# Kernel optimization log

Hardware: AMD Instinct MI355X
Metric: run time of the kernel (lower is better)

Reference implementation:

```python
import jax, jax.numpy as jnp
import numpy as np

STRIDE = 2
PAD = 1


def _deform_conv2d(x, offset, mask, weight, bias):
    # Modulated deformable conv2d (torchvision semantics), offset_groups=1,
    # stride=2, padding=1, dilation=1, groups=1.
    B, C, H, W = x.shape
    Cout, Cin, kH, kW = weight.shape
    K = kH * kW
    _, _, Ho, Wo = mask.shape

    off = offset.reshape(B, K, 2, Ho, Wo)  # [:, :, 0]=dy, [:, :, 1]=dx
    ii = jnp.repeat(jnp.arange(kH), kW).astype(x.dtype)  # [K] kernel row index
    jj = jnp.tile(jnp.arange(kW), kH).astype(x.dtype)    # [K] kernel col index
    gy = (jnp.arange(Ho) * STRIDE - PAD).astype(x.dtype)  # [Ho] base y of output pixel
    gx = (jnp.arange(Wo) * STRIDE - PAD).astype(x.dtype)  # [Wo] base x

    # Fractional sampling positions per (batch, kernel point, out pixel): [B,K,Ho,Wo]
    py = off[:, :, 0] + gy[None, None, :, None] + ii[None, :, None, None]
    px = off[:, :, 1] + gx[None, None, None, :] + jj[None, :, None, None]

    y0 = jnp.floor(py)
    x0 = jnp.floor(px)
    dy = py - y0
    dx = px - x0

    xf = x.reshape(B, C, H * W)

    def gather(yc, xc):
        # Bilinear corner gather with zero padding outside the image.
        valid = (yc >= 0) & (yc <= H - 1) & (xc >= 0) & (xc <= W - 1)
        yi = jnp.clip(yc, 0, H - 1).astype(jnp.int32)
        xi = jnp.clip(xc, 0, W - 1).astype(jnp.int32)
        idx = (yi * W + xi).reshape(B, 1, K * Ho * Wo)
        g = jnp.take_along_axis(xf, jnp.broadcast_to(idx, (B, C, K * Ho * Wo)), axis=2)
        return g.reshape(B, C, K, Ho, Wo) * valid[:, None].astype(x.dtype)

    w00 = ((1 - dy) * (1 - dx))[:, None]
    w01 = ((1 - dy) * dx)[:, None]
    w10 = (dy * (1 - dx))[:, None]
    w11 = (dy * dx)[:, None]

    val = (gather(y0, x0) * w00 + gather(y0, x0 + 1) * w01
           + gather(y0 + 1, x0) * w10 + gather(y0 + 1, x0 + 1) * w11)
    val = val * mask[:, None]  # modulation: [B,C,K,Ho,Wo] * [B,1,K,Ho,Wo]

    out = jnp.einsum('bckhw,ock->bohw', val, weight.reshape(Cout, Cin, K))
    return out + bias[None, :, None, None]


def setup_inputs() -> dict:
    key = jax.random.key(0)
    k1, k2, k3, k4, k5 = jax.random.split(key, 5)
    B, C, H, W = 8, 128, 128, 128
    Cout, kH, kW = 128, 3, 3
    Ho = (H + 2 * PAD - kH) // STRIDE + 1
    Wo = (W + 2 * PAD - kW) // STRIDE + 1
    x = jax.random.normal(k1, (B, C, H, W), dtype=jnp.float32)
    offset = jax.random.normal(k2, (B, 2 * kH * kW, Ho, Wo), dtype=jnp.float32)
    mask = jax.random.uniform(k3, (B, kH * kW, Ho, Wo), dtype=jnp.float32)
    weight = jax.random.normal(k4, (Cout, C, kH, kW), dtype=jnp.float32)
    bias = jax.random.normal(k5, (Cout,), dtype=jnp.float32)
    return {"x": x, "offset": offset, "mask": mask, "weight": weight, "bias": bias}


def reference(x, offset, mask, weight, bias):
    return _deform_conv2d(x, offset, mask, weight, bias)
```

## Files before the change

### kernel.cpp

```cpp
#include <hip/hip_runtime.h>
#include <hip/hip_bf16.h>

typedef __attribute__((ext_vector_type(8))) short short8;
typedef __attribute__((ext_vector_type(4))) short short4v;
typedef __attribute__((ext_vector_type(4))) float f32x4;
typedef __attribute__((ext_vector_type(4))) int int4v;
typedef unsigned long long u64;

#define HH 128
#define WW 128
#define CC 128
#define COUT 128
#define HO 64
#define WO 64
#define KK 9
#define PXB 64
#define NREC (KK * PXB)

__device__ __forceinline__ unsigned short bf16bits(float f) {
    union { float f; unsigned u; } u; u.f = f;
    unsigned r = u.u + 0x7fffu + ((u.u >> 16) & 1u);
    return (unsigned short)(r >> 16);
}
__device__ __forceinline__ float b2f(unsigned short h) {
    union { unsigned u; float f; } v; v.u = ((unsigned)h) << 16; return v.f;
}

__global__ void wprep_kernel(const float* __restrict__ w, unsigned short* __restrict__ wp) {
    int i = blockIdx.x * 256 + threadIdx.x;
    if (i >= KK * COUT * CC) return;
    int kp = i / (COUT * CC);
    int r = i - kp * (COUT * CC);
    int o = r >> 7;
    int c = r & 127;
    wp[i] = bf16bits(w[((size_t)o * CC + c) * KK + kp]);
}

__global__ __launch_bounds__(256, 4)
void xt_kernel(const float* __restrict__ x, unsigned short* __restrict__ xt) {
    const int bi = blockIdx.x;
    const int b = bi >> 7;
    const int y = bi & 127;
    const int t = threadIdx.x;
    __shared__ unsigned short tile[128][132];

    const float* src = x + (((size_t)b * CC) * HH + y) * WW;
#pragma unroll 8
    for (int c0 = 0; c0 < CC; c0 += 2) {
        int c = c0 + (t >> 7);
        int xx = t & 127;
        tile[xx][c] = bf16bits(src[(size_t)c * (HH * WW) + xx]);
    }
    __syncthreads();
    unsigned short* dst = xt + (((size_t)b * HH + y) * WW) * CC;
#pragma unroll
    for (int it = 0; it < 4; ++it) {
        int lin = it * 256 + t;
        int xx = lin >> 3;
        int cb = (lin & 7) * 16;
        const u64* lp = (const u64*)&tile[xx][cb];
        u64* op = (u64*)(dst + (size_t)xx * CC + cb);
        op[0] = lp[0]; op[1] = lp[1]; op[2] = lp[2]; op[3] = lp[3];
    }
}

__global__ __launch_bounds__(256, 8)
void add_kernel(float* __restrict__ out, const float* __restrict__ p1) {
    size_t i = ((size_t)blockIdx.x * 256 + threadIdx.x) * 4;
    const size_t N = (size_t)8 * COUT * HO * WO;
    const size_t STR = (size_t)2048 * 256 * 4;
    for (; i < N; i += STR) {
        f32x4 a = *(const f32x4*)(out + i);
        f32x4 b = *(const f32x4*)(p1 + i);
        a = a + b;
        *(f32x4*)(out + i) = a;
    }
}

template <bool SPLIT>
__global__ __launch_bounds__(256, 4)
void dcn14_kernel(const unsigned short* __restrict__ xt, const float* __restrict__ offset,
                  const float* __restrict__ mask, const unsigned short* __restrict__ wprep,
                  const float* __restrict__ bias, float* __restrict__ out,
                  float* __restrict__ part1) {
    const int blk = blockIdx.x;
    const int b = blk & 7;
    const int ho = (blk >> 3) & 63;
    const int chalf = SPLIT ? (blk >> 9) : 0;
    const int t = threadIdx.x;
    const int lane = t & 63;
    const int wid = t >> 6;

    __shared__ int            s_cidx[NREC][4];
    __shared__ float          s_w[NREC][4];
    __shared__ unsigned short s_val[PXB][72];

    for (int e = t; e < NREC; e += 256) {
        int kp = e >> 6;
        int wo = e & 63;
        int ky = kp / 3, kx = kp - ky * 3;
        float dy = offset[(((size_t)b * 18 + 2 * kp    ) * HO + ho) * WO + wo];
        float dx = offset[(((size_t)b * 18 + 2 * kp + 1) * HO + ho) * WO + wo];
        float m  = mask  [(((size_t)b * 9  + kp        ) * HO + ho) * WO + wo];
        float py = dy + (float)(2 * ho - 1 + ky);
        float px = dx + (float)(2 * wo - 1 + kx);
        float fy0 = floorf(py), fx0 = floorf(px);
        float ay = py - fy0, ax = px - fx0;
        int y0 = (int)fy0, x0 = (int)fx0;
        int y1 = y0 + 1, x1 = x0 + 1;
        bool vy0 = (unsigned)y0 < HH, vy1 = (unsigned)y1 < HH;
        bool vx0 = (unsigned)x0 < WW, vx1 = (unsigned)x1 < WW;
        float w00 = (vy0 && vx0) ? (1.f - ay) * (1.f - ax) * m : 0.f;
        float w01 = (vy0 && vx1) ? (1.f - ay) * ax * m : 0.f;
        float w10 = (vy1 && vx0) ? ay * (1.f - ax) * m : 0.f;
        float w11 = (vy1 && vx1) ? ay * ax * m : 0.f;
        int cy0 = min(max(y0, 0), HH - 1), cy1 = min(max(y1, 0), HH - 1);
        int cx0 = min(max(x0, 0), WW - 1), cx1 = min(max(x1, 0), WW - 1);
        s_cidx[e][0] = (cy0 * WW + cx0) * CC;
        s_cidx[e][1] = (cy0 * WW + cx1) * CC;
        s_cidx[e][2] = (cy1 * WW + cx0) * CC;
        s_cidx[e][3] = (cy1 * WW + cx1) * CC;
        s_w[e][0] = w00; s_w[e][1] = w01; s_w[e][2] = w10; s_w[e][3] = w11;
    }

    f32x4 acc[2][4];
#pragma unroll
    for (int i = 0; i < 2; ++i)
#pragma unroll
        for (int j = 0; j < 4; ++j) acc[i][j] = (f32x4){0.f, 0.f, 0.f, 0.f};

    const int o_base = wid * 32;
    const int l16 = lane & 15;
    const int lhi = lane >> 4;

    const unsigned short* xtb = xt + (size_t)b * (HH * WW * CC);
    const int gpx = t >> 2;
    const int gcb = (t & 3) * 16;

    const int cbeg = SPLIT ? chalf * 64 : 0;
    const int cend = SPLIT ? cbeg + 64 : CC;

    for (int c0 = cbeg; c0 < cend; c0 += 64) {
        for (int kp = 0; kp < KK; ++kp) {
            __syncthreads();

            int rec = kp * PXB + gpx;
            int4v ci = *(const int4v*)&s_cidx[rec][0];
            f32x4 wq = *(const f32x4*)&s_w[rec][0];
            const unsigned short* bp = xtb + c0 + gcb;
            short8 h00a = *(const short8*)(bp + ci.x);
            short8 h00b = *(const short8*)(bp + ci.x + 8);
            short8 h01a = *(const short8*)(bp + ci.y);
            short8 h01b = *(const short8*)(bp + ci.y + 8);
            short8 h10a = *(const short8*)(bp + ci.z);
            short8 h10b = *(const short8*)(bp + ci.z + 8);
            short8 h11a = *(const short8*)(bp + ci.w);
            short8 h11b = *(const short8*)(bp + ci.w + 8);

            const unsigned short* wb = wprep + (size_t)kp * (COUT * CC) + c0 + lhi * 8;
            short8 afr[2][2];
#pragma unroll
            for (int mr = 0; mr < 2; ++mr)
#pragma unroll
                for (int kk = 0; kk < 2; ++kk)
                    afr[mr][kk] = *(const short8*)(wb + (size_t)(o_base + mr * 16 + l16) * CC + kk * 32);

            short8 v0, v1;
#pragma unroll
            for (int j = 0; j < 8; ++j) {
                float val = wq.x * b2f((unsigned short)h00a[j]) + wq.y * b2f((unsigned short)h01a[j])
                          + wq.z * b2f((unsigned short)h10a[j]) + wq.w * b2f((unsigned short)h11a[j]);
                v0[j] = (short)bf16bits(val);
            }
#pragma unroll
            for (int j = 0; j < 8; ++j) {
                float val = wq.x * b2f((unsigned short)h00b[j]) + wq.y * b2f((unsigned short)h01b[j])
                          + wq.z * b2f((unsigned short)h10b[j]) + wq.w * b2f((unsigned short)h11b[j]);
                v1[j] = (short)bf16bits(val);
            }
            *(short8*)&s_val[gpx][gcb] = v0;
            *(short8*)&s_val[gpx][gcb + 8] = v1;

            __syncthreads();

#pragma unroll
            for (int nr = 0; nr < 4; ++nr) {
                short8 bfr[2];
#pragma unroll
                for (int kk = 0; kk < 2; ++kk)
                    bfr[kk] = *(const short8*)&s_val[nr * 16 + l16][kk * 32 + lhi * 8];
#pragma unroll
                for (int mr = 0; mr < 2; ++mr)
#pragma unroll
                    for (int kk = 0; kk < 2; ++kk)
                        acc[mr][nr] = __builtin_amdgcn_mfma_f32_16x16x32_bf16(
                            afr[mr][kk], bfr[kk], acc[mr][nr], 0, 0, 0);
            }
        }
    }

    float* dst = (SPLIT && chalf == 1) ? part1 : out;
    const bool addb = (!SPLIT) || (chalf == 0);
    float* ob = dst + ((size_t)b * COUT) * (HO * WO) + (size_t)ho * WO;
#pragma unroll
    for (int mr = 0; mr < 2; ++mr) {
        int o_r = o_base + mr * 16 + lhi * 4;
#pragma unroll
        for (int r = 0; r < 4; ++r) {
            int o = o_r + r;
            float bs = addb ? bias[o] : 0.f;
#pragma unroll
            for (int nr = 0; nr < 4; ++nr) {
                int wo = nr * 16 + l16;
                ob[(size_t)o * (HO * WO) + wo] = acc[mr][nr][r] + bs;
            }
        }
    }
}

#define PXB6 32
#define NREC6 (KK * PXB6)
template <bool PREP>
__global__ __launch_bounds__(256, 4)
void dcn6_kernel(const float* __restrict__ x, const float* __restrict__ offset,
                 const float* __restrict__ mask, const float* __restrict__ weight,
                 const unsigned short* __restrict__ wprep,
                 const float* __restrict__ bias, float* __restrict__ out) {
    const int blk = blockIdx.x;
    const int b = blk & 7;
    const int rr = blk >> 3;
    const int ho = rr >> 1;
    const int px0 = (rr & 1) * PXB6;
    const int t = threadIdx.x;
    const int lane = t & 63;
    const int wid = t >> 6;

    __shared__ int            s_off[NREC6][2];
    __shared__ float          s_wq[NREC6][4];
    __shared__ unsigned short s_wt6[COUT][40];
    __shared__ unsigned short s_val6[PXB6][40];

    for (int e = t; e < NREC6; e += 256) {
        int kp = e >> 5;
        int wo = px0 + (e & 31);
        int ky = kp / 3, kx = kp - ky * 3;
        float dy = offset[(((size_t)b * 18 + 2 * kp    ) * HO + ho) * WO + wo];
        float dx = offset[(((size_t)b * 18 + 2 * kp + 1) * HO + ho) * WO + wo];
        float m  = mask  [(((size_t)b * 9  + kp        ) * HO + ho) * WO + wo];
        float py = dy + (float)(2 * ho - 1 + ky);
        float px = dx + (float)(2 * wo - 1 + kx);
        float fy0 = floorf(py), fx0 = floorf(px);
        float ay = py - fy0, ax = px - fx0;
        int y0 = (int)fy0, x0 = (int)fx0;
        int y1 = y0 + 1, x1 = x0 + 1;
        bool vy0 = (unsigned)y0 < HH, vy1 = (unsigned)y1 < HH;
        bool vx0 = (unsigned)x0 < WW, vx1 = (unsigned)x1 < WW;
        float w00 = (vy0 && vx0) ? (1.f - ay) * (1.f - ax) * m : 0.f;
        float w01 = (vy0 && vx1) ? (1.f - ay) * ax * m : 0.f;
        float w10 = (vy1 && vx0) ? ay * (1.f - ax) * m : 0.f;
        float w11 = (vy1 && vx1) ? ay * ax * m : 0.f;
        int bx = min(max(x0, 0), WW - 2);
        float wA0 = (x0 == bx     ? w00 : 0.f) + (x1 == bx     ? w01 : 0.f);
        float wB0 = (x0 == bx + 1 ? w00 : 0.f) + (x1 == bx + 1 ? w01 : 0.f);
        float wA1 = (x0 == bx     ? w10 : 0.f) + (x1 == bx     ? w11 : 0.f);
        float wB1 = (x0 == bx + 1 ? w10 : 0.f) + (x1 == bx + 1 ? w11 : 0.f);
        int cy0 = min(max(y0, 0), HH - 1), cy1 = min(max(y1, 0), HH - 1);
        s_off[e][0] = cy0 * WW + bx;
        s_off[e][1] = cy1 * WW + bx;
        s_wq[e][0] = wA0; s_wq[e][1] = wB0; s_wq[e][2] = wA1; s_wq[e][3] = wB1;
    }

    f32x4 acc[2][2];
#pragma unroll
    for (int i = 0; i < 2; ++i)
#pragma unroll
        for (int j = 0; j < 2; ++j) acc[i][j] = (f32x4){0.f, 0.f, 0.f, 0.f};

    const int o_base = wid * 32;
    const int l16 = lane & 15;
    const int lhi = lane >> 4;
    const float* xb = x + (size_t)b * CC * HH * WW;
    const int gpx = t & 31;
    const int gcg = t >> 5;

    for (int c0 = 0; c0 < CC; c0 += 32) {
        for (int kp = 0; kp < KK; ++kp) {
            __syncthreads();
            if (PREP) {
                const unsigned short* src =
                    wprep + ((size_t)kp * COUT + (t >> 1)) * CC + c0 + (t & 1) * 16;
                short8 w0 = *(const short8*)(src);
                short8 w1 = *(const short8*)(src + 8);
                *(short8*)&s_wt6[t >> 1][(t & 1) * 16] = w0;
                *(short8*)&s_wt6[t >> 1][(t & 1) * 16 + 8] = w1;
            } else {
                int o = t & 127;
                int clb = (t >> 7) * 16;
                const float* wp = weight + (size_t)o * (CC * KK) + (size_t)(c0 + clb) * KK + kp;
                short8 w0, w1;
#pragma unroll
                for (int j = 0; j < 8; ++j) w0[j] = (short)bf16bits(wp[j * KK]);
#pragma unroll
                for (int j = 0; j < 8; ++j) w1[j] = (short)bf16bits(wp[(8 + j) * KK]);
                *(short8*)&s_wt6[o][clb] = w0;
                *(short8*)&s_wt6[o][clb + 8] = w1;
            }
            {
                int rec = kp * PXB6 + gpx;
                int o0 = s_off[rec][0], o1 = s_off[rec][1];
                f32x4 wq = *(const f32x4*)&s_wq[rec][0];
                const float* pl = xb + (size_t)(c0 + gcg * 4) * (HH * WW);
                short4v v;
#pragma unroll
                for (int j = 0; j < 4; ++j) {
                    const float* p = pl + (size_t)j * (HH * WW);
                    float2 f0 = *(const float2*)(p + o0);
                    float2 f1 = *(const float2*)(p + o1);
                    float val = wq.x * f0.x + wq.y * f0.y + wq.z * f1.x + wq.w * f1.y;
                    v[j] = (short)bf16bits(val);
                }
                *(short4v*)&s_val6[gpx][gcg * 4] = v;
            }
            __syncthreads();
            short8 afr[2];
#pragma unroll
            for (int mr = 0; mr < 2; ++mr)
                afr[mr] = *(const short8*)&s_wt6[o_base + mr * 16 + l16][lhi * 8];
            short8 bfr[2];
#pragma unroll
            for (int nr = 0; nr < 2; ++nr)
                bfr[nr] = *(const short8*)&s_val6[nr * 16 + l16][lhi * 8];
#pragma unroll
            for (int mr = 0; mr < 2; ++mr)
#pragma unroll
                for (int nr = 0; nr < 2; ++nr)
                    acc[mr][nr] = __builtin_amdgcn_mfma_f32_16x16x32_bf16(
                        afr[mr], bfr[nr], acc[mr][nr], 0, 0, 0);
        }
    }

    float* ob = out + ((size_t)b * COUT) * (HO * WO) + (size_t)ho * WO;
#pragma unroll
    for (int mr = 0; mr < 2; ++mr) {
        int o_r = o_base + mr * 16 + lhi * 4;
#pragma unroll
        for (int r = 0; r < 4; ++r) {
            int o = o_r + r;
            float bs = bias[o];
#pragma unroll
            for (int nr = 0; nr < 2; ++nr) {
                int wo = px0 + nr * 16 + l16;
                ob[(size_t)o * (HO * WO) + wo] = acc[mr][nr][r] + bs;
            }
        }
    }
}

extern "C" void kernel_launch(void* const* d_in, const int* in_sizes, int n_in,
                              void* d_out, int out_size, void* d_ws, size_t ws_size,
                              hipStream_t stream) {
    (void)in_sizes; (void)n_in; (void)out_size;
    const float* x      = (const float*)d_in[0];
    const float* offset = (const float*)d_in[1];
    const float* mask   = (const float*)d_in[2];
    const float* weight = (const float*)d_in[3];
    const float* bias   = (const float*)d_in[4];
    float* out = (float*)d_out;

    const size_t wbytes  = (size_t)KK * COUT * CC * sizeof(unsigned short);
    const size_t xtoff   = (size_t)1 << 20;
    const size_t xtbytes = (size_t)8 * HH * WW * CC * sizeof(unsigned short);
    const size_t p1off   = xtoff + xtbytes;
    const size_t p1bytes = (size_t)8 * COUT * HO * WO * sizeof(float);

    if (ws_size >= p1off + p1bytes) {
        unsigned short* wp  = (unsigned short*)d_ws;
        unsigned short* xtp = (unsigned short*)((char*)d_ws + xtoff);
        float* p1           = (float*)((char*)d_ws + p1off);
        wprep_kernel<<<dim3((KK * COUT * CC + 255) / 256), dim3(256), 0, stream>>>(weight, wp);
        xt_kernel<<<dim3(1024), dim3(256), 0, stream>>>(x, xtp);
        dcn14_kernel<true><<<dim3(1024), dim3(256), 0, stream>>>(xtp, offset, mask, wp, bias, out, p1);
        add_kernel<<<dim3(2048), dim3(256), 0, stream>>>(out, p1);
    } else if (ws_size >= xtoff + xtbytes) {
        unsigned short* wp  = (unsigned short*)d_ws;
        unsigned short* xtp = (unsigned short*)((char*)d_ws + xtoff);
        wprep_kernel<<<dim3((KK * COUT * CC + 255) / 256), dim3(256), 0, stream>>>(weight, wp);
        xt_kernel<<<dim3(1024), dim3(256), 0, stream>>>(x, xtp);
        dcn14_kernel<false><<<dim3(512), dim3(256), 0, stream>>>(xtp, offset, mask, wp, bias, out, nullptr);
    } else if (ws_size >= wbytes) {
        unsigned short* wp = (unsigned short*)d_ws;
        wprep_kernel<<<dim3((KK * COUT * CC + 255) / 256), dim3(256), 0, stream>>>(weight, wp);
        dcn6_kernel<true><<<dim3(1024), dim3(256), 0, stream>>>(x, offset, mask, weight, wp, bias, out);
    } else {
        dcn6_kernel<false><<<dim3(1024), dim3(256), 0, stream>>>(x, offset, mask, weight, nullptr, bias, out);
    }
}
```

Before: 70.50 us.

## Merge prep kernels and replace partial-sum add pass with atomic accumulation

Folds the weight conversion, x transpose, and zeroing of the output into a single prep launch. The split-channel DCN kernel then accumulates both channel halves directly into the output with float atomicAdd, which removes the separate partial buffer and the add kernel. This cuts two launches and a full read/write pass over the output. In exchange it adds an explicit zero-fill of the output, atomic traffic, and nondeterministic summation order. The wprep fallback path is also changed to use the unprepared dcn6 variant.

```diff
diff --git a/kernel.cpp b/kernel.cpp
--- a/kernel.cpp
+++ b/kernel.cpp
@@ -26,63 +26,58 @@
     union { unsigned u; float f; } v; v.u = ((unsigned)h) << 16; return v.f;
 }
 
-__global__ void wprep_kernel(const float* __restrict__ w, unsigned short* __restrict__ wp) {
-    int i = blockIdx.x * 256 + threadIdx.x;
-    if (i >= KK * COUT * CC) return;
-    int kp = i / (COUT * CC);
-    int r = i - kp * (COUT * CC);
-    int o = r >> 7;
-    int c = r & 127;
-    wp[i] = bf16bits(w[((size_t)o * CC + c) * KK + kp]);
-}
-
 __global__ __launch_bounds__(256, 4)
-void xt_kernel(const float* __restrict__ x, unsigned short* __restrict__ xt) {
-    const int bi = blockIdx.x;
-    const int b = bi >> 7;
-    const int y = bi & 127;
+void prep_kernel(const float* __restrict__ x, unsigned short* __restrict__ xt,
+                 const float* __restrict__ w, unsigned short* __restrict__ wp,
+                 float* __restrict__ out) {
+    const int blk = blockIdx.x;
     const int t = threadIdx.x;
     __shared__ unsigned short tile[128][132];
 
-    const float* src = x + (((size_t)b * CC) * HH + y) * WW;
+    if (blk < 1024) {
+        const int b = blk >> 7;
+        const int y = blk & 127;
+        const float* src = x + (((size_t)b * CC) * HH + y) * WW;
 #pragma unroll 8
-    for (int c0 = 0; c0 < CC; c0 += 2) {
-        int c = c0 + (t >> 7);
-        int xx = t & 127;
-        tile[xx][c] = bf16bits(src[(size_t)c * (HH * WW) + xx]);
-    }
-    __syncthreads();
-    unsigned short* dst = xt + (((size_t)b * HH + y) * WW) * CC;
-#pragma unroll
-    for (int it = 0; it < 4; ++it) {
-        int lin = it * 256 + t;
-        int xx = lin >> 3;
-        int cb = (lin & 7) * 16;
-        const u64* lp = (const u64*)&tile[xx][cb];
-        u64* op = (u64*)(dst + (size_t)xx * CC + cb);
-        op[0] = lp[0]; op[1] = lp[1]; op[2] = lp[2]; op[3] = lp[3];
-    }
-}
-
-__global__ __launch_bounds__(256, 8)
-void add_kernel(float* __restrict__ out, const float* __restrict__ p1) {
-    size_t i = ((size_t)blockIdx.x * 256 + threadIdx.x) * 4;
-    const size_t N = (size_t)8 * COUT * HO * WO;
-    const size_t STR = (size_t)2048 * 256 * 4;
-    for (; i < N; i += STR) {
-        f32x4 a = *(const f32x4*)(out + i);
-        f32x4 b = *(const f32x4*)(p1 + i);
-        a = a + b;
-        *(f32x4*)(out + i) = a;
+        for (int c0 = 0; c0 < CC; c0 += 2) {
+            int c = c0 + (t >> 7);
+            int xx = t & 127;
+            tile[xx][c] = bf16bits(src[(size_t)c * (HH * WW) + xx]);
+        }
+        __syncthreads();
+        unsigned short* dst = xt + (((size_t)b * HH + y) * WW) * CC;
+#pragma unroll
+        for (int it = 0; it < 4; ++it) {
+            int lin = it * 256 + t;
+            int xx = lin >> 3;
+            int cb = (lin & 7) * 16;
+            const u64* lp = (const u64*)&tile[xx][cb];
+            u64* op = (u64*)(dst + (size_t)xx * CC + cb);
+            op[0] = lp[0]; op[1] = lp[1]; op[2] = lp[2]; op[3] = lp[3];
+        }
+    } else if (blk < 1600) {
+        int i = (blk - 1024) * 256 + t;
+        if (i < KK * COUT * CC) {
+            int kp = i / (COUT * CC);
+            int r = i - kp * (COUT * CC);
+            int o = r >> 7;
+            int c = r & 127;
+            wp[i] = bf16bits(w[((size_t)o * CC + c) * KK + kp]);
+        }
+    } else {
+        f32x4* o4 = (f32x4*)out;
+        size_t idx = (size_t)(blk - 1600) * 256 + t;
+#pragma unroll
+        for (int k = 0; k < 16; ++k)
+            o4[idx + (size_t)k * 65536] = (f32x4){0.f, 0.f, 0.f, 0.f};
     }
 }
 
 template <bool SPLIT>
 __global__ __launch_bounds__(256, 4)
-void dcn14_kernel(const unsigned short* __restrict__ xt, const float* __restrict__ offset,
+void dcn15_kernel(const unsigned short* __restrict__ xt, const float* __restrict__ offset,
                   const float* __restrict__ mask, const unsigned short* __restrict__ wprep,
-                  const float* __restrict__ bias, float* __restrict__ out,
-                  float* __restrict__ part1) {
+                  const float* __restrict__ bias, float* __restrict__ out) {
     const int blk = blockIdx.x;
     const int b = blk & 7;
     const int ho = (blk >> 3) & 63;
@@ -199,20 +194,35 @@
         }
     }
 
-    float* dst = (SPLIT && chalf == 1) ? part1 : out;
-    const bool addb = (!SPLIT) || (chalf == 0);
-    float* ob = dst + ((size_t)b * COUT) * (HO * WO) + (size_t)ho * WO;
-#pragma unroll
-    for (int mr = 0; mr < 2; ++mr) {
-        int o_r = o_base + mr * 16 + lhi * 4;
-#pragma unroll
-        for (int r = 0; r < 4; ++r) {
-            int o = o_r + r;
-            float bs = addb ? bias[o] : 0.f;
-#pragma unroll
-            for (int nr = 0; nr < 4; ++nr) {
-                int wo = nr * 16 + l16;
-                ob[(size_t)o * (HO * WO) + wo] = acc[mr][nr][r] + bs;
+    float* ob = out + ((size_t)b * COUT) * (HO * WO) + (size_t)ho * WO;
+    if (SPLIT) {
+#pragma unroll
+        for (int mr = 0; mr < 2; ++mr) {
+            int o_r = o_base + mr * 16 + lhi * 4;
+#pragma unroll
+            for (int r = 0; r < 4; ++r) {
+                int o = o_r + r;
+                float bs = (chalf == 0) ? bias[o] : 0.f;
+#pragma unroll
+                for (int nr = 0; nr < 4; ++nr) {
+                    int wo = nr * 16 + l16;
+                    atomicAdd(&ob[(size_t)o * (HO * WO) + wo], acc[mr][nr][r] + bs);
+                }
+            }
+        }
+    } else {
+#pragma unroll
+        for (int mr = 0; mr < 2; ++mr) {
+            int o_r = o_base + mr * 16 + lhi * 4;
+#pragma unroll
+            for (int r = 0; r < 4; ++r) {
+                int o = o_r + r;
+                float bs = bias[o];
+#pragma unroll
+                for (int nr = 0; nr < 4; ++nr) {
+                    int wo = nr * 16 + l16;
+                    ob[(size_t)o * (HO * WO) + wo] = acc[mr][nr][r] + bs;
+                }
             }
         }
     }
@@ -370,27 +380,15 @@
     const size_t wbytes  = (size_t)KK * COUT * CC * sizeof(unsigned short);
     const size_t xtoff   = (size_t)1 << 20;
     const size_t xtbytes = (size_t)8 * HH * WW * CC * sizeof(unsigned short);
-    const size_t p1off   = xtoff + xtbytes;
-    const size_t p1bytes = (size_t)8 * COUT * HO * WO * sizeof(float);
-
-    if (ws_size >= p1off + p1bytes) {
+
+    if (ws_size >= xtoff + xtbytes) {
         unsigned short* wp  = (unsigned short*)d_ws;
         unsigned short* xtp = (unsigned short*)((char*)d_ws + xtoff);
-        float* p1           = (float*)((char*)d_ws + p1off);
-        wprep_kernel<<<dim3((KK * COUT * CC + 255) / 256), dim3(256), 0, stream>>>(weight, wp);
-        xt_kernel<<<dim3(1024), dim3(256), 0, stream>>>(x, xtp);
-        dcn14_kernel<true><<<dim3(1024), dim3(256), 0, stream>>>(xtp, offset, mask, wp, bias, out, p1);
-        add_kernel<<<dim3(2048), dim3(256), 0, stream>>>(out, p1);
-    } else if (ws_size >= xtoff + xtbytes) {
-        unsigned short* wp  = (unsigned short*)d_ws;
-        unsigned short* xtp = (unsigned short*)((char*)d_ws + xtoff);
-        wprep_kernel<<<dim3((KK * COUT * CC + 255) / 256), dim3(256), 0, stream>>>(weight, wp);
-        xt_kernel<<<dim3(1024), dim3(256), 0, stream>>>(x, xtp);
-        dcn14_kernel<false><<<dim3(512), dim3(256), 0, stream>>>(xtp, offset, mask, wp, bias, out, nullptr);
+        prep_kernel<<<dim3(1856), dim3(256), 0, stream>>>(x, xtp, weight, wp, out);
+        dcn15_kernel<true><<<dim3(1024), dim3(256), 0, stream>>>(xtp, offset, mask, wp, bias, out);
     } else if (ws_size >= wbytes) {
         unsigned short* wp = (unsigned short*)d_ws;
-        wprep_kernel<<<dim3((KK * COUT * CC + 255) / 256), dim3(256), 0, stream>>>(weight, wp);
-        dcn6_kernel<true><<<dim3(1024), dim3(256), 0, stream>>>(x, offset, mask, weight, wp, bias, out);
+        dcn6_kernel<false><<<dim3(1024), dim3(256), 0, stream>>>(x, offset, mask, weight, nullptr, bias, out);
     } else {
         dcn6_kernel<false><<<dim3(1024), dim3(256), 0, stream>>>(x, offset, mask, weight, nullptr, bias, out);
     }
```

Result: no change. 69.68 us (-1.2%).
